# Performance work log

Measured on AMD Instinct MI355X. Metric: run time of the kernel, lower is better.

The kernel has to match this reference:

```python
import jax, jax.numpy as jnp
import numpy as np

B, N, M, C, H = 8, 2048, 1024, 512, 8
D = C // H  # per-head dim = 64


def setup_inputs() -> dict:
    key = jax.random.key(0)
    ks = jax.random.split(key, 4)
    x = jax.random.normal(ks[0], (B, N, C), dtype=jnp.float32)
    global_tokens = jax.random.normal(ks[1], (B, M, C), dtype=jnp.float32)
    Wq = jax.random.normal(ks[2], (C, C), dtype=jnp.float32) * 0.02
    bq = jnp.zeros((C,), dtype=jnp.float32)
    Wkv = jax.random.normal(ks[3], (C, 2 * C), dtype=jnp.float32) * 0.02
    bkv = jnp.zeros((2 * C,), dtype=jnp.float32)
    return {"x": x, "global_tokens": global_tokens, "Wq": Wq, "bq": bq,
            "Wkv": Wkv, "bkv": bkv}


def reference(x, global_tokens, Wq, bq, Wkv, bkv):
    # q from x, k/v from global_tokens (LinearProjection with query=True)
    q = (x @ Wq + bq).reshape(B, N, H, D).transpose(0, 2, 1, 3)        # [B,H,N,D]
    kv = (global_tokens @ Wkv + bkv).reshape(B, M, 2, H, D)
    k = kv[:, :, 0].transpose(0, 2, 1, 3)                              # [B,H,M,D]
    v = kv[:, :, 1].transpose(0, 2, 1, 3)                              # [B,H,M,D]
    # NOTE: original module applies no 1/sqrt(D) scaling in forward
    attn = jnp.einsum('bhnd,bhmd->bhnm', q, k)                         # [B,H,N,M]
    attn = jax.nn.softmax(attn, axis=-1)
    out = jnp.einsum('bhnm,bhmd->bhnd', attn, v)                       # [B,H,N,D]
    return out.transpose(0, 2, 1, 3).reshape(B, N, C)
```

## Files before the change

kernel.cpp:

```cpp
#include <hip/hip_runtime.h>
#include <hip/hip_bf16.h>


typedef __bf16 bf16_t;
typedef __bf16 bf16x8 __attribute__((ext_vector_type(8)));
typedef __bf16 bf16x4 __attribute__((ext_vector_type(4)));
typedef float floatx16 __attribute__((ext_vector_type(16)));
typedef unsigned int uintx4 __attribute__((ext_vector_type(4)));
typedef unsigned int uintx2 __attribute__((ext_vector_type(2)));

#define KDIM 512
#define QSCALE 1.44269504088896f

#define WAITVM(N) asm volatile("s_waitcnt vmcnt(" #N ")" ::: "memory")
#define BAR()                                  \
  do {                                         \
    __builtin_amdgcn_s_barrier();              \
    asm volatile("" ::: "memory");             \
  } while (0)

__device__ __forceinline__ unsigned pack2(float a, float b) {
  unsigned short ua = __builtin_bit_cast(unsigned short, (bf16_t)a);
  unsigned short ub = __builtin_bit_cast(unsigned short, (bf16_t)b);
  return (unsigned)ua | ((unsigned)ub << 16);
}

__device__ __forceinline__ float fexp2(float x) {
#if __has_builtin(__builtin_amdgcn_exp2f)
  return __builtin_amdgcn_exp2f(x);
#else
  return __exp2f(x);
#endif
}

__device__ __forceinline__ bf16x8 cvt8(const float4 a, const float4 b) {
  bf16x8 r;
  r[0] = (bf16_t)a.x; r[1] = (bf16_t)a.y; r[2] = (bf16_t)a.z; r[3] = (bf16_t)a.w;
  r[4] = (bf16_t)b.x; r[5] = (bf16_t)b.y; r[6] = (bf16_t)b.z; r[7] = (bf16_t)b.w;
  return r;
}

__device__ __forceinline__ void gl_lds16(const bf16_t* g, bf16_t* l) {
#if __has_builtin(__builtin_amdgcn_global_load_lds)
  __builtin_amdgcn_global_load_lds(
      (const __attribute__((address_space(1))) unsigned int*)(g),
      (__attribute__((address_space(3))) unsigned int*)(l), 16, 0, 0);
#else
  *(bf16x8*)l = *(const bf16x8*)g;
#endif
}

__global__ __launch_bounds__(256) void prep_kernel(
    const float* __restrict__ Wq, const float* __restrict__ Wkv,
    const float* __restrict__ x, const float* __restrict__ gt,
    bf16_t* __restrict__ Wqt, bf16_t* __restrict__ Wkvt,
    bf16_t* __restrict__ Aq, bf16_t* __restrict__ Akv) {
  __shared__ float tile[64][65];
  const int blk = blockIdx.x;
  const int t = threadIdx.x;
  if (blk < 192) {
    const float* in; bf16_t* out; int N, bx, by;
    if (blk < 64) { in = Wq; out = Wqt; N = 512; bx = blk & 7; by = blk >> 3; }
    else { int t2 = blk - 64; in = Wkv; out = Wkvt; N = 1024; bx = t2 & 15; by = t2 >> 4; }
    const int c0 = bx * 64, k0 = by * 64;
#pragma unroll
    for (int i = 0; i < 16; ++i) {
      int idx = t + i * 256;
      int kk = idx >> 6, cc = idx & 63;
      tile[kk][cc] = in[(size_t)(k0 + kk) * N + (c0 + cc)];
    }
    __syncthreads();
#pragma unroll
    for (int j = 0; j < 2; ++j) {
      int unit = t + j * 256;
      int cc = unit >> 3, ks = (unit & 7) * 8;
      int c = c0 + cc, k = k0 + ks;
      bf16x8 v;
#pragma unroll
      for (int i = 0; i < 8; ++i) v[i] = (bf16_t)tile[ks + i][cc];
      const int k5 = k & 31;
      const int chunk = ((c & 127) >> 5) * 2 + (k5 >> 4);
      *(bf16x8*)(&out[(size_t)((c >> 7) * 16 + (k >> 5)) * 4096 + chunk * 512 +
                      (c & 31) * 8 + ((k5 >> 3) & 1) * 256]) = v;
    }
  } else {
    int idx = blk - 192;
    const float* src; bf16_t* dst; int rt, kt2;
    if (idx < 2048) { src = x; dst = Aq; rt = idx >> 4; kt2 = idx & 15; }
    else { int i2 = idx - 2048; src = gt; dst = Akv; rt = i2 >> 4; kt2 = i2 & 15; }
    const int row = rt * 128 + (t >> 1);
    const int kb = kt2 * 32 + (t & 1) * 16;
    const float* p = src + (size_t)row * KDIM + kb;
    float4 f0 = *(const float4*)(p);
    float4 f1 = *(const float4*)(p + 4);
    float4 f2 = *(const float4*)(p + 8);
    float4 f3 = *(const float4*)(p + 12);
    bf16x8 o0 = cvt8(f0, f1), o1 = cvt8(f2, f3);
    const int chunk = ((row & 127) >> 5) * 2 + (t & 1);
    bf16_t* ob = dst + (size_t)(rt * 16 + kt2) * 4096 + chunk * 512 + (row & 31) * 8;
    *(bf16x8*)(ob) = o0;
    *(bf16x8*)(ob + 256) = o1;
  }
}

__global__ __launch_bounds__(256) void proj_gemm_kernel(
    const bf16_t* __restrict__ Aq, const bf16_t* __restrict__ Akv,
    const bf16_t* __restrict__ Wqt, const bf16_t* __restrict__ Wkvt,
    const float* __restrict__ bq, const float* __restrict__ bkv,
    bf16_t* __restrict__ Qf, bf16_t* __restrict__ Kf, bf16_t* __restrict__ Vf) {
  __shared__ bf16_t lds[2][8192];
  const int raw = blockIdx.x;
  const int blk = (raw & 7) * 128 + (raw >> 3);
  int mode, bx, by;
  const bf16_t* Ab; const bf16_t* Wb; const float* bias;
  if (blk < 512) { mode = 0; bx = blk & 3; by = blk >> 2; Ab = Aq; Wb = Wqt; bias = bq; }
  else { int tt = blk - 512; mode = 1; bx = tt & 7; by = tt >> 3; Ab = Akv; Wb = Wkvt; bias = bkv; }

  const int tid = threadIdx.x;
  const int wave = tid >> 6, L = tid & 63;
  const int l5 = L & 31, hf = L >> 5;
  const int wr = wave >> 1, wc = wave & 1;
  const int rb = by * 128, cb = bx * 128;

  const bf16_t* Abase = Ab + (size_t)by * 16 * 4096 + L * 8;
  const bf16_t* Wbase = Wb + (size_t)bx * 16 * 4096 + L * 8;

  auto dma = [&](int buf, int kt) {
#pragma unroll
    for (int j = 0; j < 4; ++j) {
      const int s = wave * 4 + j;
      const bf16_t* g = (s < 8) ? (Abase + (size_t)kt * 4096 + s * 512)
                                : (Wbase + (size_t)kt * 4096 + (s - 8) * 512);
      gl_lds16(g, &lds[buf][(s < 8 ? s * 512 : 4096 + (s - 8) * 512) + L * 8]);
    }
  };

  dma(0, 0);
  __syncthreads();

  floatx16 acc[2][2] = {};
  for (int kt = 0; kt < 16; ++kt) {
    const int cur = kt & 1;
    if (kt < 15) dma(cur ^ 1, kt + 1);
    bf16x8 af[2][2], wf[2][2];
#pragma unroll
    for (int rs = 0; rs < 2; ++rs)
#pragma unroll
      for (int kh = 0; kh < 2; ++kh)
        af[rs][kh] = *(const bf16x8*)(&lds[cur][((wr * 2 + rs) * 2 + kh) * 512 + L * 8]);
#pragma unroll
    for (int cs = 0; cs < 2; ++cs)
#pragma unroll
      for (int kh = 0; kh < 2; ++kh)
        wf[cs][kh] = *(const bf16x8*)(&lds[cur][4096 + ((wc * 2 + cs) * 2 + kh) * 512 + L * 8]);
    __builtin_amdgcn_s_setprio(1);
#pragma unroll
    for (int rs = 0; rs < 2; ++rs)
#pragma unroll
      for (int cs = 0; cs < 2; ++cs)
#pragma unroll
        for (int kh = 0; kh < 2; ++kh)
          acc[rs][cs] = __builtin_amdgcn_mfma_f32_32x32x16_bf16(
              af[rs][kh], wf[cs][kh], acc[rs][cs], 0, 0, 0);
    __builtin_amdgcn_s_setprio(0);
    __syncthreads();
  }

  const int colb = cb + wc * 64;
  char* stc = (char*)(&lds[0][0] + wave * 4096);
  const int gr0 = rb + wr * 64;

  if (mode == 0 || colb < 512) {
    bf16_t* dstT; size_t base2;
    const int hh = (colb & 511) >> 6;
    if (mode == 0) {
      const int b = gr0 >> 11, n0 = gr0 & 2047;
      base2 = 2 * ((size_t)(b * 8 + hh) * 131072 + (size_t)(n0 >> 5) * 2048);
      dstT = Qf;
    } else {
      const int b = gr0 >> 10, m0 = gr0 & 1023;
      base2 = 2 * ((size_t)(b * 8 + hh) * 65536 + (size_t)(m0 >> 5) * 2048);
      dstT = Kf;
    }
#pragma unroll
    for (int rs = 0; rs < 2; ++rs)
#pragma unroll
      for (int cs = 0; cs < 2; ++cs) {
        const int d = cs * 32 + l5;
        const float bv = bias[colb + cs * 32 + l5];
#pragma unroll
        for (int r = 0; r < 16; ++r) {
          const int nl = rs * 32 + (r & 3) + 8 * (r >> 2) + 4 * hf;
          float v = acc[rs][cs][r] + bv;
          if (mode == 0) v *= QSCALE;
          int q = ((nl >> 5) << 12) | ((d >> 3) << 9) | ((nl & 31) << 4) | ((d & 7) << 1);
          q ^= ((q >> 9) & 7) << 4;
          *(bf16_t*)(stc + q) = (bf16_t)v;
        }
      }
#pragma unroll
    for (int g = 0; g < 8; ++g) {
      const int q = g * 1024 + L * 16;
      const int qs = q ^ (((q >> 9) & 7) << 4);
      bf16x8 vv = *(const bf16x8*)(stc + qs);
      *(bf16x8*)((char*)dstT + base2 + q) = vv;
    }
  } else {
#pragma unroll
    for (int rs = 0; rs < 2; ++rs)
#pragma unroll
      for (int cs = 0; cs < 2; ++cs) {
        const int col = colb + cs * 32 + l5;
        const float bv = bias[col];
        const int grb = gr0 + rs * 32;
        const int cc = col - 512;
        const int hh = cc >> 6, d = cc & 63;
        const int dof = (d >> 5) * 1024 + (d & 31) * 8;
#pragma unroll
        for (int rq = 0; rq < 4; ++rq) {
          int gr = grb + 8 * rq + 4 * hf;
          int b = gr >> 10, m = gr & 1023;
          bf16x4 pk;
          pk[0] = (bf16_t)(acc[rs][cs][rq * 4 + 0] + bv);
          pk[1] = (bf16_t)(acc[rs][cs][rq * 4 + 1] + bv);
          pk[2] = (bf16_t)(acc[rs][cs][rq * 4 + 2] + bv);
          pk[3] = (bf16_t)(acc[rs][cs][rq * 4 + 3] + bv);
          *(bf16x4*)(&Vf[(size_t)(b * 8 + hh) * 65536 + (m >> 5) * 2048 + dof +
                         ((m >> 4) & 1) * 512 + ((m >> 3) & 1) * 256 + (m & 7)]) = pk;
        }
      }
  }
}

__global__ __launch_bounds__(256, 4) void flash_attn_kernel(
    const bf16_t* __restrict__ Qf, const bf16_t* __restrict__ Kf,
    const bf16_t* __restrict__ Vf, float* __restrict__ out) {
  __shared__ bf16_t kv[4][4096];
  const int tid = threadIdx.x;
  const int wave = tid >> 6, L = tid & 63;
  const int l5 = L & 31, hf = L >> 5;
  const int bh = blockIdx.y;
  const int b = bh >> 3, hh = bh & 7;
  const int nb = blockIdx.x * 128 + wave * 32;

  const bf16_t* Qp = Qf + (size_t)bh * 131072 + (nb >> 5) * 2048 + L * 8;
  const bf16_t* Kb = Kf + (size_t)bh * 65536 + L * 8;
  const bf16_t* Vb = Vf + (size_t)bh * 65536 + L * 8;

  bf16x8 qf[4];
#pragma unroll
  for (int kc = 0; kc < 4; ++kc) qf[kc] = *(const bf16x8*)(Qp + kc * 512);

  bf16x8 ones;
#pragma unroll
  for (int i = 0; i < 8; ++i) ones[i] = (bf16_t)1.0f;

  floatx16 o0 = {}, o1 = {}, lacc = {};

  auto dma = [&](int buf, int s) {
#pragma unroll
    for (int j = 0; j < 2; ++j) {
      const int q = wave * 2 + j;
      const bf16_t* g = (q < 4) ? (Kb + (size_t)s * 2048 + q * 512)
                                : (Vb + (size_t)s * 2048 + (q - 4) * 512);
      gl_lds16(g, &kv[buf][(q < 4 ? q * 512 : 2048 + (q - 4) * 512) + L * 8]);
    }
  };

  auto subtile = [&](int s) {
    const bf16_t* kb = &kv[s & 3][L * 8];
    const bf16_t* vb = &kv[s & 3][2048 + L * 8];
    bf16x8 kf4[4];
#pragma unroll
    for (int kc = 0; kc < 4; ++kc) kf4[kc] = *(const bf16x8*)(kb + kc * 512);
    floatx16 sa = {};
    __builtin_amdgcn_s_setprio(1);
#pragma unroll
    for (int kc = 0; kc < 4; ++kc)
      sa = __builtin_amdgcn_mfma_f32_32x32x16_bf16(kf4[kc], qf[kc], sa, 0, 0, 0);
    __builtin_amdgcn_s_setprio(0);
    bf16x8 vf4[4];
#pragma unroll
    for (int j = 0; j < 4; ++j) vf4[j] = *(const bf16x8*)(vb + j * 512);
    unsigned w[8];
#pragma unroll
    for (int i = 0; i < 8; ++i) {
      float pa = fexp2(sa[2 * i]), pb = fexp2(sa[2 * i + 1]);
      w[i] = pack2(pa, pb);
    }
    uintx4 fw0, fw1;
#if __has_builtin(__builtin_amdgcn_permlane32_swap)
    {
      uintx2 r0 = __builtin_amdgcn_permlane32_swap(w[0], w[2], false, false);
      uintx2 r1 = __builtin_amdgcn_permlane32_swap(w[1], w[3], false, false);
      uintx2 r2 = __builtin_amdgcn_permlane32_swap(w[4], w[6], false, false);
      uintx2 r3 = __builtin_amdgcn_permlane32_swap(w[5], w[7], false, false);
      fw0.x = r0[0]; fw0.z = r0[1];
      fw0.y = r1[0]; fw0.w = r1[1];
      fw1.x = r2[0]; fw1.z = r2[1];
      fw1.y = r3[0]; fw1.w = r3[1];
    }
#else
    {
      unsigned sw[8];
#pragma unroll
      for (int i = 0; i < 8; ++i) sw[i] = __shfl_xor(w[i], 32);
      fw0.x = hf ? sw[2] : w[0]; fw0.y = hf ? sw[3] : w[1];
      fw0.z = hf ? w[2] : sw[0]; fw0.w = hf ? w[3] : sw[1];
      fw1.x = hf ? sw[6] : w[4]; fw1.y = hf ? sw[7] : w[5];
      fw1.z = hf ? w[6] : sw[4]; fw1.w = hf ? w[7] : sw[5];
    }
#endif
    bf16x8 pf0 = __builtin_bit_cast(bf16x8, fw0);
    bf16x8 pf1 = __builtin_bit_cast(bf16x8, fw1);
    __builtin_amdgcn_s_setprio(1);
    lacc = __builtin_amdgcn_mfma_f32_32x32x16_bf16(ones, pf0, lacc, 0, 0, 0);
    lacc = __builtin_amdgcn_mfma_f32_32x32x16_bf16(ones, pf1, lacc, 0, 0, 0);
    o0 = __builtin_amdgcn_mfma_f32_32x32x16_bf16(vf4[0], pf0, o0, 0, 0, 0);
    o0 = __builtin_amdgcn_mfma_f32_32x32x16_bf16(vf4[1], pf1, o0, 0, 0, 0);
    o1 = __builtin_amdgcn_mfma_f32_32x32x16_bf16(vf4[2], pf0, o1, 0, 0, 0);
    o1 = __builtin_amdgcn_mfma_f32_32x32x16_bf16(vf4[3], pf1, o1, 0, 0, 0);
    __builtin_amdgcn_s_setprio(0);
  };

  dma(0, 0);
  dma(1, 1);
  dma(2, 2);

  for (int s = 0; s < 30; ++s) {
    WAITVM(4);
    BAR();
    if (s <= 28) dma((s + 3) & 3, s + 3);
    subtile(s);
  }
  WAITVM(2);
  BAR();
  subtile(30);
  WAITVM(0);
  BAR();
  subtile(31);

  __syncthreads();

  const float inv = 1.0f / lacc[0];

  float* lob = (float*)(&kv[0][0]) + wave * (32 * 36);
  const size_t orow = (size_t)b * 2048 + nb;
#pragma unroll
  for (int pass = 0; pass < 2; ++pass) {
    const floatx16& oo = pass ? o1 : o0;
#pragma unroll
    for (int i = 0; i < 8; ++i) {
      const int d = 2 * (i & 1) + 8 * (i >> 1) + 4 * hf;
      float2 a;
      a.x = oo[2 * i] * inv; a.y = oo[2 * i + 1] * inv;
      *(float2*)(&lob[l5 * 36 + d]) = a;
    }
#pragma unroll
    for (int j = 0; j < 4; ++j) {
      int chunk = j * 64 + L;
      int n = chunk >> 3, c = chunk & 7;
      float4 v = *(const float4*)(&lob[n * 36 + c * 4]);
      *(float4*)(&out[(orow + n) * 512 + hh * 64 + pass * 32 + c * 4]) = v;
    }
  }
}

extern "C" void kernel_launch(void* const* d_in, const int* in_sizes, int n_in,
                              void* d_out, int out_size, void* d_ws, size_t ws_size,
                              hipStream_t stream) {
  (void)in_sizes; (void)n_in; (void)out_size; (void)ws_size;
  const float* x   = (const float*)d_in[0];
  const float* gt  = (const float*)d_in[1];
  const float* Wq  = (const float*)d_in[2];
  const float* bq  = (const float*)d_in[3];
  const float* Wkv = (const float*)d_in[4];
  const float* bkv = (const float*)d_in[5];
  float* out = (float*)d_out;

  bf16_t* Wqt  = (bf16_t*)d_ws;
  bf16_t* Wkvt = Wqt + (size_t)512 * 512;
  bf16_t* Qf   = Wkvt + (size_t)1024 * 512;
  bf16_t* Kf   = Qf + (size_t)64 * 2048 * 64;
  bf16_t* Vf   = Kf + (size_t)64 * 1024 * 64;
  bf16_t* Aq   = (bf16_t*)d_out;
  bf16_t* Akv  = Aq + (size_t)16384 * 512;

  prep_kernel<<<3264, 256, 0, stream>>>(Wq, Wkv, x, gt, Wqt, Wkvt, Aq, Akv);
  proj_gemm_kernel<<<1024, 256, 0, stream>>>(Aq, Akv, Wqt, Wkvt, bq, bkv, Qf, Kf, Vf);
  flash_attn_kernel<<<dim3(16, 64), 256, 0, stream>>>(Qf, Kf, Vf, out);
}
```

Before: 174.8 us.

## Load projection GEMM operands directly from global into registers, dropping LDS staging

The projection GEMM no longer stages A and W tiles through double-buffered shared memory with barriers. Each wave loads its MFMA fragments straight from the pre-swizzled global layout into registers, ping-ponging two register sets across k-steps. This removes the LDS round trip and the per-iteration block barrier. In exchange, operands shared between waves are fetched redundantly from global memory or L2, and register pressure rises.

Measured after the change: 180.0 us. 1.03x slower.

```diff
diff --git a/kernel.cpp b/kernel.cpp
--- a/kernel.cpp
+++ b/kernel.cpp
@@ -108,7 +108,7 @@
     const bf16_t* __restrict__ Wqt, const bf16_t* __restrict__ Wkvt,
     const float* __restrict__ bq, const float* __restrict__ bkv,
     bf16_t* __restrict__ Qf, bf16_t* __restrict__ Kf, bf16_t* __restrict__ Vf) {
-  __shared__ bf16_t lds[2][8192];
+  __shared__ bf16_t lds[16384];
   const int raw = blockIdx.x;
   const int blk = (raw & 7) * 128 + (raw >> 3);
   int mode, bx, by;
@@ -122,37 +122,32 @@
   const int wr = wave >> 1, wc = wave & 1;
   const int rb = by * 128, cb = bx * 128;
 
-  const bf16_t* Abase = Ab + (size_t)by * 16 * 4096 + L * 8;
-  const bf16_t* Wbase = Wb + (size_t)bx * 16 * 4096 + L * 8;
-
-  auto dma = [&](int buf, int kt) {
-#pragma unroll
-    for (int j = 0; j < 4; ++j) {
-      const int s = wave * 4 + j;
-      const bf16_t* g = (s < 8) ? (Abase + (size_t)kt * 4096 + s * 512)
-                                : (Wbase + (size_t)kt * 4096 + (s - 8) * 512);
-      gl_lds16(g, &lds[buf][(s < 8 ? s * 512 : 4096 + (s - 8) * 512) + L * 8]);
-    }
+  const bf16_t* pA = Ab + (size_t)by * 65536 + L * 8;
+  const bf16_t* pW = Wb + (size_t)bx * 65536 + L * 8;
+
+  auto ldA = [&](int kt, int rs, int kh) {
+    return *(const bf16x8*)(pA + kt * 4096 + ((wr * 2 + rs) * 2 + kh) * 512);
   };
-
-  dma(0, 0);
-  __syncthreads();
+  auto ldW = [&](int kt, int cs, int kh) {
+    return *(const bf16x8*)(pW + kt * 4096 + ((wc * 2 + cs) * 2 + kh) * 512);
+  };
 
   floatx16 acc[2][2] = {};
-  for (int kt = 0; kt < 16; ++kt) {
-    const int cur = kt & 1;
-    if (kt < 15) dma(cur ^ 1, kt + 1);
-    bf16x8 af[2][2], wf[2][2];
+  bf16x8 a0[2][2], w0[2][2], a1[2][2], w1[2][2];
+
+#pragma unroll
+  for (int rs = 0; rs < 2; ++rs)
+#pragma unroll
+    for (int kh = 0; kh < 2; ++kh) { a0[rs][kh] = ldA(0, rs, kh); w0[rs][kh] = ldW(0, rs, kh); }
+
+  for (int kt = 0; kt < 16; kt += 2) {
 #pragma unroll
     for (int rs = 0; rs < 2; ++rs)
 #pragma unroll
-      for (int kh = 0; kh < 2; ++kh)
-        af[rs][kh] = *(const bf16x8*)(&lds[cur][((wr * 2 + rs) * 2 + kh) * 512 + L * 8]);
-#pragma unroll
-    for (int cs = 0; cs < 2; ++cs)
-#pragma unroll
-      for (int kh = 0; kh < 2; ++kh)
-        wf[cs][kh] = *(const bf16x8*)(&lds[cur][4096 + ((wc * 2 + cs) * 2 + kh) * 512 + L * 8]);
+      for (int kh = 0; kh < 2; ++kh) {
+        a1[rs][kh] = ldA(kt + 1, rs, kh);
+        w1[rs][kh] = ldW(kt + 1, rs, kh);
+      }
     __builtin_amdgcn_s_setprio(1);
 #pragma unroll
     for (int rs = 0; rs < 2; ++rs)
@@ -161,13 +156,31 @@
 #pragma unroll
         for (int kh = 0; kh < 2; ++kh)
           acc[rs][cs] = __builtin_amdgcn_mfma_f32_32x32x16_bf16(
-              af[rs][kh], wf[cs][kh], acc[rs][cs], 0, 0, 0);
+              a0[rs][kh], w0[cs][kh], acc[rs][cs], 0, 0, 0);
     __builtin_amdgcn_s_setprio(0);
-    __syncthreads();
+    if (kt + 2 < 16) {
+#pragma unroll
+      for (int rs = 0; rs < 2; ++rs)
+#pragma unroll
+        for (int kh = 0; kh < 2; ++kh) {
+          a0[rs][kh] = ldA(kt + 2, rs, kh);
+          w0[rs][kh] = ldW(kt + 2, rs, kh);
+        }
+    }
+    __builtin_amdgcn_s_setprio(1);
+#pragma unroll
+    for (int rs = 0; rs < 2; ++rs)
+#pragma unroll
+      for (int cs = 0; cs < 2; ++cs)
+#pragma unroll
+        for (int kh = 0; kh < 2; ++kh)
+          acc[rs][cs] = __builtin_amdgcn_mfma_f32_32x32x16_bf16(
+              a1[rs][kh], w1[cs][kh], acc[rs][cs], 0, 0, 0);
+    __builtin_amdgcn_s_setprio(0);
   }
 
   const int colb = cb + wc * 64;
-  char* stc = (char*)(&lds[0][0] + wave * 4096);
+  char* stc = (char*)(lds + wave * 4096);
   const int gr0 = rb + wr * 64;
 
   if (mode == 0 || colb < 512) {
```

## Fuse fp32-to-bf16 activation conversion into projection GEMM A-tile loads

Applied to the files above, without the earlier changes.

The prep kernel no longer converts x and global_tokens to bf16 in a staging buffer. Instead the projection GEMM loads fp32 A tiles straight into registers, converts them, and writes them into LDS in the MFMA-friendly layout. Only the weight tiles still go through the async global-to-LDS path. This removes a full write and re-read of the bf16 activation copy and shrinks the prep launch, but the A-tile path now moves twice the bytes in fp32 and adds register-staged conversion and LDS writes inside the GEMM main loop.

Result: slower. 186.4 us (+6.6%).

```diff
diff --git a/kernel.cpp b/kernel.cpp
--- a/kernel.cpp
+++ b/kernel.cpp
@@ -37,6 +37,12 @@
   bf16x8 r;
   r[0] = (bf16_t)a.x; r[1] = (bf16_t)a.y; r[2] = (bf16_t)a.z; r[3] = (bf16_t)a.w;
   r[4] = (bf16_t)b.x; r[5] = (bf16_t)b.y; r[6] = (bf16_t)b.z; r[7] = (bf16_t)b.w;
+  return r;
+}
+
+__device__ __forceinline__ bf16x4 cvt4(const float4 a) {
+  bf16x4 r;
+  r[0] = (bf16_t)a.x; r[1] = (bf16_t)a.y; r[2] = (bf16_t)a.z; r[3] = (bf16_t)a.w;
   return r;
 }
 
@@ -52,59 +58,38 @@
 
 __global__ __launch_bounds__(256) void prep_kernel(
     const float* __restrict__ Wq, const float* __restrict__ Wkv,
-    const float* __restrict__ x, const float* __restrict__ gt,
-    bf16_t* __restrict__ Wqt, bf16_t* __restrict__ Wkvt,
-    bf16_t* __restrict__ Aq, bf16_t* __restrict__ Akv) {
+    bf16_t* __restrict__ Wqt, bf16_t* __restrict__ Wkvt) {
   __shared__ float tile[64][65];
   const int blk = blockIdx.x;
   const int t = threadIdx.x;
-  if (blk < 192) {
-    const float* in; bf16_t* out; int N, bx, by;
-    if (blk < 64) { in = Wq; out = Wqt; N = 512; bx = blk & 7; by = blk >> 3; }
-    else { int t2 = blk - 64; in = Wkv; out = Wkvt; N = 1024; bx = t2 & 15; by = t2 >> 4; }
-    const int c0 = bx * 64, k0 = by * 64;
-#pragma unroll
-    for (int i = 0; i < 16; ++i) {
-      int idx = t + i * 256;
-      int kk = idx >> 6, cc = idx & 63;
-      tile[kk][cc] = in[(size_t)(k0 + kk) * N + (c0 + cc)];
-    }
-    __syncthreads();
-#pragma unroll
-    for (int j = 0; j < 2; ++j) {
-      int unit = t + j * 256;
-      int cc = unit >> 3, ks = (unit & 7) * 8;
-      int c = c0 + cc, k = k0 + ks;
-      bf16x8 v;
-#pragma unroll
-      for (int i = 0; i < 8; ++i) v[i] = (bf16_t)tile[ks + i][cc];
-      const int k5 = k & 31;
-      const int chunk = ((c & 127) >> 5) * 2 + (k5 >> 4);
-      *(bf16x8*)(&out[(size_t)((c >> 7) * 16 + (k >> 5)) * 4096 + chunk * 512 +
-                      (c & 31) * 8 + ((k5 >> 3) & 1) * 256]) = v;
-    }
-  } else {
-    int idx = blk - 192;
-    const float* src; bf16_t* dst; int rt, kt2;
-    if (idx < 2048) { src = x; dst = Aq; rt = idx >> 4; kt2 = idx & 15; }
-    else { int i2 = idx - 2048; src = gt; dst = Akv; rt = i2 >> 4; kt2 = i2 & 15; }
-    const int row = rt * 128 + (t >> 1);
-    const int kb = kt2 * 32 + (t & 1) * 16;
-    const float* p = src + (size_t)row * KDIM + kb;
-    float4 f0 = *(const float4*)(p);
-    float4 f1 = *(const float4*)(p + 4);
-    float4 f2 = *(const float4*)(p + 8);
-    float4 f3 = *(const float4*)(p + 12);
-    bf16x8 o0 = cvt8(f0, f1), o1 = cvt8(f2, f3);
-    const int chunk = ((row & 127) >> 5) * 2 + (t & 1);
-    bf16_t* ob = dst + (size_t)(rt * 16 + kt2) * 4096 + chunk * 512 + (row & 31) * 8;
-    *(bf16x8*)(ob) = o0;
-    *(bf16x8*)(ob + 256) = o1;
+  const float* in; bf16_t* out; int N, bx, by;
+  if (blk < 64) { in = Wq; out = Wqt; N = 512; bx = blk & 7; by = blk >> 3; }
+  else { int t2 = blk - 64; in = Wkv; out = Wkvt; N = 1024; bx = t2 & 15; by = t2 >> 4; }
+  const int c0 = bx * 64, k0 = by * 64;
+#pragma unroll
+  for (int i = 0; i < 16; ++i) {
+    int idx = t + i * 256;
+    int kk = idx >> 6, cc = idx & 63;
+    tile[kk][cc] = in[(size_t)(k0 + kk) * N + (c0 + cc)];
+  }
+  __syncthreads();
+#pragma unroll
+  for (int j = 0; j < 2; ++j) {
+    int unit = t + j * 256;
+    int cc = unit >> 3, ks = (unit & 7) * 8;
+    int c = c0 + cc, k = k0 + ks;
+    bf16x8 v;
+#pragma unroll
+    for (int i = 0; i < 8; ++i) v[i] = (bf16_t)tile[ks + i][cc];
+    const int k5 = k & 31;
+    const int chunk = ((c & 127) >> 5) * 2 + (k5 >> 4);
+    *(bf16x8*)(&out[(size_t)((c >> 7) * 16 + (k >> 5)) * 4096 + chunk * 512 +
+                    (c & 31) * 8 + ((k5 >> 3) & 1) * 256]) = v;
   }
 }
 
 __global__ __launch_bounds__(256) void proj_gemm_kernel(
-    const bf16_t* __restrict__ Aq, const bf16_t* __restrict__ Akv,
+    const float* __restrict__ x, const float* __restrict__ gt,
     const bf16_t* __restrict__ Wqt, const bf16_t* __restrict__ Wkvt,
     const float* __restrict__ bq, const float* __restrict__ bkv,
     bf16_t* __restrict__ Qf, bf16_t* __restrict__ Kf, bf16_t* __restrict__ Vf) {
@@ -112,9 +97,9 @@
   const int raw = blockIdx.x;
   const int blk = (raw & 7) * 128 + (raw >> 3);
   int mode, bx, by;
-  const bf16_t* Ab; const bf16_t* Wb; const float* bias;
-  if (blk < 512) { mode = 0; bx = blk & 3; by = blk >> 2; Ab = Aq; Wb = Wqt; bias = bq; }
-  else { int tt = blk - 512; mode = 1; bx = tt & 7; by = tt >> 3; Ab = Akv; Wb = Wkvt; bias = bkv; }
+  const float* Asrc; const bf16_t* Wb; const float* bias;
+  if (blk < 512) { mode = 0; bx = blk & 3; by = blk >> 2; Asrc = x; Wb = Wqt; bias = bq; }
+  else { int tt = blk - 512; mode = 1; bx = tt & 7; by = tt >> 3; Asrc = gt; Wb = Wkvt; bias = bkv; }
 
   const int tid = threadIdx.x;
   const int wave = tid >> 6, L = tid & 63;
@@ -122,26 +107,44 @@
   const int wr = wave >> 1, wc = wave & 1;
   const int rb = by * 128, cb = bx * 128;
 
-  const bf16_t* Abase = Ab + (size_t)by * 16 * 4096 + L * 8;
+  const float* abase = Asrc + (size_t)(rb + 32 * wave + (L >> 3)) * KDIM + (L & 7) * 4;
+  const int u = L & 7;
+  const int aoff0 = (wave * 2 + (u >> 2)) * 512 + (L >> 3) * 8 +
+                    ((u >> 1) & 1) * 256 + (u & 1) * 4;
+
+  float4 av[4];
+  auto loadA = [&](int kt) {
+#pragma unroll
+    for (int j = 0; j < 4; ++j)
+      av[j] = *(const float4*)(abase + (size_t)(8 * j) * KDIM + kt * 32);
+  };
+  auto writeA = [&](int buf) {
+#pragma unroll
+    for (int j = 0; j < 4; ++j)
+      *(bf16x4*)(&lds[buf][aoff0 + j * 64]) = cvt4(av[j]);
+  };
+
   const bf16_t* Wbase = Wb + (size_t)bx * 16 * 4096 + L * 8;
-
-  auto dma = [&](int buf, int kt) {
-#pragma unroll
-    for (int j = 0; j < 4; ++j) {
-      const int s = wave * 4 + j;
-      const bf16_t* g = (s < 8) ? (Abase + (size_t)kt * 4096 + s * 512)
-                                : (Wbase + (size_t)kt * 4096 + (s - 8) * 512);
-      gl_lds16(g, &lds[buf][(s < 8 ? s * 512 : 4096 + (s - 8) * 512) + L * 8]);
-    }
-  };
-
-  dma(0, 0);
+  auto dmaW = [&](int buf, int kt) {
+#pragma unroll
+    for (int j = 0; j < 2; ++j) {
+      const int s = wave * 2 + j;
+      gl_lds16(Wbase + (size_t)kt * 4096 + s * 512, &lds[buf][4096 + s * 512 + L * 8]);
+    }
+  };
+
+  loadA(0);
+  dmaW(0, 0);
+  writeA(0);
   __syncthreads();
 
   floatx16 acc[2][2] = {};
   for (int kt = 0; kt < 16; ++kt) {
     const int cur = kt & 1;
-    if (kt < 15) dma(cur ^ 1, kt + 1);
+    if (kt < 15) {
+      loadA(kt + 1);
+      dmaW(cur ^ 1, kt + 1);
+    }
     bf16x8 af[2][2], wf[2][2];
 #pragma unroll
     for (int rs = 0; rs < 2; ++rs)
@@ -163,6 +166,7 @@
           acc[rs][cs] = __builtin_amdgcn_mfma_f32_32x32x16_bf16(
               af[rs][kh], wf[cs][kh], acc[rs][cs], 0, 0, 0);
     __builtin_amdgcn_s_setprio(0);
+    if (kt < 15) writeA(cur ^ 1);
     __syncthreads();
   }
 
@@ -383,10 +387,8 @@
   bf16_t* Qf   = Wkvt + (size_t)1024 * 512;
   bf16_t* Kf   = Qf + (size_t)64 * 2048 * 64;
   bf16_t* Vf   = Kf + (size_t)64 * 1024 * 64;
-  bf16_t* Aq   = (bf16_t*)d_out;
-  bf16_t* Akv  = Aq + (size_t)16384 * 512;
-
-  prep_kernel<<<3264, 256, 0, stream>>>(Wq, Wkv, x, gt, Wqt, Wkvt, Aq, Akv);
-  proj_gemm_kernel<<<1024, 256, 0, stream>>>(Aq, Akv, Wqt, Wkvt, bq, bkv, Qf, Kf, Vf);
+
+  prep_kernel<<<192, 256, 0, stream>>>(Wq, Wkv, Wqt, Wkvt);
+  proj_gemm_kernel<<<1024, 256, 0, stream>>>(x, gt, Wqt, Wkvt, bq, bkv, Qf, Kf, Vf);
   flash_attn_kernel<<<dim3(16, 64), 256, 0, stream>>>(Qf, Kf, Vf, out);
 }
```
